# Kernel optimization log

Measured on AMD Instinct MI355X. Metric: run time of the kernel, lower is better.

Reference implementation:

```python
import jax, jax.numpy as jnp
import numpy as np

N_HEAD = 12
N_EMBD = 768

def setup_inputs() -> dict:
    key = jax.random.key(0)
    k1, k2, k3 = jax.random.split(key, 3)
    B, T, C = 4, 2048, N_EMBD
    x = jax.random.normal(k1, (B, T, C), dtype=jnp.float32)
    w_attn = jax.random.normal(k2, (C, 3 * C), dtype=jnp.float32) * (C ** -0.5)
    b_attn = jnp.zeros((3 * C,), dtype=jnp.float32)
    w_proj = jax.random.normal(k3, (C, C), dtype=jnp.float32) * (C ** -0.5)
    b_proj = jnp.zeros((C,), dtype=jnp.float32)
    return {"x": x, "w_attn": w_attn, "b_attn": b_attn, "w_proj": w_proj, "b_proj": b_proj}

def reference(x, w_attn, b_attn, w_proj, b_proj):
    B, T, C = x.shape
    H = N_HEAD
    D = C // H
    qkv = x @ w_attn + b_attn  # [B,T,3C]
    q, k, v = jnp.split(qkv, 3, axis=-1)
    # [B,H,T,D]
    q = q.reshape(B, T, H, D).transpose(0, 2, 1, 3)
    k = k.reshape(B, T, H, D).transpose(0, 2, 1, 3)
    v = v.reshape(B, T, H, D).transpose(0, 2, 1, 3)
    # NOTE: source scales by n_embd**-0.5, not head_dim**-0.5
    scores = jnp.einsum('bhqd,bhkd->bhqk', q, k) * (C ** -0.5)
    causal = jnp.triu(jnp.ones((T, T), dtype=bool), k=1)  # True above diagonal
    scores = jnp.where(causal, -jnp.inf, scores)
    attn = jax.nn.softmax(scores, axis=-1)
    out = jnp.einsum('bhqk,bhkd->bhqd', attn, v)  # [B,H,T,D]
    out = out.transpose(0, 2, 1, 3).reshape(B, T, C)
    return out @ w_proj + b_proj
```

## Files before the change

kernel.cpp:

```cpp
#include <hip/hip_runtime.h>
#include <cstdint>
#include <cstddef>

typedef __attribute__((ext_vector_type(8))) short bf8_t;
typedef __attribute__((ext_vector_type(4))) float f4_t;
typedef __attribute__((ext_vector_type(16))) float f16v_t;
typedef __attribute__((ext_vector_type(2))) unsigned u2_t;
typedef __attribute__((ext_vector_type(4))) unsigned u4_t;

#define DEVFN static __device__ __forceinline__
#define MFMA16(a, b, c) __builtin_amdgcn_mfma_f32_16x16x32_bf16(a, b, c, 0, 0, 0)
#define MFMA32(a, b, c) __builtin_amdgcn_mfma_f32_32x32x16_bf16(a, b, c, 0, 0, 0)

constexpr float kQscale = 0.05205877317700523f;

DEVFN short f2bs(float f) {
  uint32_t u = __builtin_bit_cast(uint32_t, f);
  u = (u + 0x7FFFu + ((u >> 16) & 1u)) >> 16;
  return (short)(uint16_t)u;
}

DEVFN unsigned cvtpk(float lo, float hi) {
  unsigned r;
  asm("v_cvt_pk_bf16_f32 %0, %1, %2" : "=v"(r) : "v"(lo), "v"(hi));
  return r;
}

DEVFN float red2_sum(float v) { return v + __shfl_xor(v, 32, 64); }

DEVFN void gload16(const void* g, void* l) {
  __builtin_amdgcn_global_load_lds(
      (const __attribute__((address_space(1))) void*)g,
      (__attribute__((address_space(3))) void*)l, 16, 0, 0);
}

__global__ __launch_bounds__(256) void prep(const float* __restrict__ x,
                                            short* __restrict__ xb,
                                            const float* __restrict__ w_attn,
                                            short* __restrict__ wat,
                                            const float* __restrict__ w_proj,
                                            short* __restrict__ wpt) {
  __shared__ float tile[32][33];
  const int blk = blockIdx.x, tid = threadIdx.x;
  if (blk < 3072) {
    const int i = blk * 256 + tid;
    const f4_t* p = (const f4_t*)x + (size_t)i * 2;
    f4_t a = p[0], b = p[1];
    bf8_t h;
    h[0] = f2bs(a[0]); h[1] = f2bs(a[1]); h[2] = f2bs(a[2]); h[3] = f2bs(a[3]);
    h[4] = f2bs(b[0]); h[5] = f2bs(b[1]); h[6] = f2bs(b[2]); h[7] = f2bs(b[3]);
    *((bf8_t*)xb + i) = h;
    return;
  }
  const float* w;
  short* wT;
  int N, n0, k0;
  if (blk < 4800) {
    const int bb = blk - 3072;
    w = w_attn; wT = wat; N = 2304;
    n0 = (bb % 72) << 5; k0 = (bb / 72) << 5;
  } else {
    const int bb = blk - 4800;
    w = w_proj; wT = wpt; N = 768;
    n0 = (bb % 24) << 5; k0 = (bb / 24) << 5;
  }
  const int tx = tid & 31, ty = tid >> 5;
#pragma unroll
  for (int i = 0; i < 4; ++i)
    tile[ty * 4 + i][tx] = w[(size_t)(k0 + ty * 4 + i) * N + n0 + tx];
  __syncthreads();
#pragma unroll
  for (int i = 0; i < 4; ++i)
    wT[(size_t)(n0 + ty * 4 + i) * 768 + k0 + tx] = f2bs(tile[tx][ty * 4 + i]);
}

template <int EPI, int BN, int NW>
__global__ __launch_bounds__(NW * 64) void gemm_bf16(
    const short* __restrict__ A, const short* __restrict__ Bt,
    const float* __restrict__ bias, float* __restrict__ outF,
    short* __restrict__ qb, short* __restrict__ kb, short* __restrict__ vtb,
    int Mdim, int Ndim, int Kdim) {
  constexpr int NT = NW * 64;
  constexpr int WCN = NW / 2;
  constexpr int WNW = BN / WCN;
  constexpr int NI = WNW / 16;
  constexpr int ACH = 16 / NW;
  constexpr int BCH = BN / (8 * NW);
  __shared__ char smem[32768 + (BN << 7)];
  const int nbx = gridDim.x;
  const int bid = blockIdx.x + nbx * blockIdx.y;
  const int xcd = bid & 7, slot = bid >> 3;
  const int mp = xcd + ((slot / nbx) << 3);
  const int np = slot % nbx;
  const int m0 = mp << 7, n0 = np * BN;
  const int tid = threadIdx.x;
  const int lane = tid & 63, wid = tid >> 6;
  const int wr = wid / WCN, wc = wid % WCN;
  const int g = lane >> 4, cl = lane & 15;
  const int ldb = Kdim << 1;

  f4_t acc[4][NI];
#pragma unroll
  for (int mi = 0; mi < 4; ++mi)
#pragma unroll
    for (int ni = 0; ni < NI; ++ni) acc[mi][ni] = (f4_t){0.f, 0.f, 0.f, 0.f};

  const char* ga = (const char*)(A + (size_t)m0 * Kdim);
  const char* gb = (const char*)(Bt + (size_t)n0 * Kdim);
  auto stageA = [&](int b, int ks) {
    const int k0b = ks << 7;
    char* Ab = smem + (b << 14);
#pragma unroll
    for (int i = 0; i < ACH; ++i) {
      const int doff = (wid * ACH + i) << 10;
      const int boff = doff + lane * 16;
      const int row = boff >> 7;
      const int src = row * ldb + k0b + ((boff & 127) ^ ((row & 7) << 4));
      gload16(ga + src, Ab + doff);
    }
  };
  auto stageB = [&](int ks) {
    const int k0b = ks << 7;
    char* Bb = smem + 32768;
#pragma unroll
    for (int i = 0; i < BCH; ++i) {
      const int doff = (wid * BCH + i) << 10;
      const int boff = doff + lane * 16;
      const int row = boff >> 7;
      const int src = row * ldb + k0b + ((boff & 127) ^ ((row & 7) << 4));
      gload16(gb + src, Bb + doff);
    }
  };

  const int nk = Kdim >> 6;
  stageA(0, 0);
  stageB(0);
  __syncthreads();

  int cur = 0;
  for (int ks = 0; ks < nk; ++ks) {
    const int ksn = (ks + 1 < nk) ? ks + 1 : ks;
    const char* Ab = smem + (cur << 14);
    const char* Bb = smem + 32768;
    bf8_t bfv[2][NI], af0[4];
#pragma unroll
    for (int kk = 0; kk < 2; ++kk)
#pragma unroll
      for (int ni = 0; ni < NI; ++ni) {
        int lrow = wc * WNW + (ni << 4) + cl;
        bfv[kk][ni] = *(const bf8_t*)&Bb[(lrow << 7) + ((((kk << 2) + g) ^ (lrow & 7)) << 4)];
      }
#pragma unroll
    for (int mi = 0; mi < 4; ++mi) {
      int lrow = (wr << 6) + (mi << 4) + cl;
      af0[mi] = *(const bf8_t*)&Ab[(lrow << 7) + (((g) ^ (lrow & 7)) << 4)];
    }
    __syncthreads();
    stageA(cur ^ 1, ksn);
    stageB(ksn);
#pragma unroll
    for (int mi = 0; mi < 4; ++mi)
#pragma unroll
      for (int ni = 0; ni < NI; ++ni)
        acc[mi][ni] = MFMA16(af0[mi], bfv[0][ni], acc[mi][ni]);
    bf8_t af1[4];
#pragma unroll
    for (int mi = 0; mi < 4; ++mi) {
      int lrow = (wr << 6) + (mi << 4) + cl;
      af1[mi] = *(const bf8_t*)&Ab[(lrow << 7) + (((4 + g) ^ (lrow & 7)) << 4)];
    }
#pragma unroll
    for (int mi = 0; mi < 4; ++mi)
#pragma unroll
      for (int ni = 0; ni < NI; ++ni)
        acc[mi][ni] = MFMA16(af1[mi], bfv[1][ni], acc[mi][ni]);
    __syncthreads();
    cur ^= 1;
  }

  if constexpr (EPI == 1) {
#pragma unroll
    for (int ni = 0; ni < NI; ++ni) {
      const int n = n0 + wc * WNW + (ni << 4) + cl;
      const float bv = bias[n];
#pragma unroll
      for (int mi = 0; mi < 4; ++mi)
#pragma unroll
        for (int r = 0; r < 4; ++r) {
          const int m = m0 + (wr << 6) + (mi << 4) + (g << 2) + r;
          outF[(size_t)m * 768 + n] = acc[mi][ni][r] + bv;
        }
    }
  } else {
    short* T = (short*)smem;
    const int sec = n0 / 768;
    const float qs = (sec == 0) ? kQscale : 1.0f;
#pragma unroll
    for (int ni = 0; ni < NI; ++ni) {
      const int colT = wc * WNW + (ni << 4) + cl;
      const float bv = bias[n0 + colT];
#pragma unroll
      for (int mi = 0; mi < 4; ++mi)
#pragma unroll
        for (int r = 0; r < 4; ++r) {
          const int row = (wr << 6) + (mi << 4) + (g << 2) + r;
          const int colS = ((((colT >> 3) ^ ((row >> 3) & 7)) << 3) | (colT & 7));
          T[row * 132 + colS] = f2bs((acc[mi][ni][r] + bv) * qs);
        }
    }
    __syncthreads();
    if (sec < 2) {
      short* dst0 = (sec == 0) ? qb : kb;
      const int tl = tid & 127;
      const int hh2 = (tid >> 7) & 1;
      const int half = tid >> 8;
      constexpr int JN = (NT == 256) ? 8 : 4;
      const int m = m0 + tl, b = m >> 11, t = m & 2047;
      const int hh = ((n0 - sec * 768) >> 6) + hh2;
      short* dst = dst0 + (size_t)(b * 12 + hh) * 131072 + (size_t)t * 64 + half * 32;
      const int rsw = (tl >> 3) & 7;
#pragma unroll
      for (int j = 0; j < JN; ++j) {
        const int gj = (hh2 << 3) + (half << 2) + j;
        *(bf8_t*)(dst + j * 8) =
            *(const bf8_t*)(T + tl * 132 + ((gj ^ rsw) << 3));
      }
    } else {
      const int chunk = tid & 15;
      constexpr int DLS = NT >> 4;
      const int m = m0 + (chunk << 3);
      const int b = m >> 11, t = m & 2047;
#pragma unroll
      for (int c8 = 0; c8 < 128 / DLS; ++c8) {
        const int dl = (tid >> 4) + c8 * DLS;
        const int nloc = n0 - 1536 + dl;
        const int hh = nloc >> 6, d = nloc & 63;
        const int gsw = ((dl >> 3) ^ (chunk & 7)) << 3;
        bf8_t tmp;
#pragma unroll
        for (int j = 0; j < 8; ++j)
          tmp[j] = T[((chunk << 3) + j) * 132 + gsw + (dl & 7)];
        *(bf8_t*)(vtb + (size_t)(b * 12 + hh) * 131072 + (size_t)d * 2048 + t) = tmp;
      }
    }
  }
}

__global__ __launch_bounds__(256, 2) void attn_fwd(const short* __restrict__ Q,
                                                   const short* __restrict__ K,
                                                   const short* __restrict__ Vt,
                                                   short* __restrict__ O) {
  __shared__ char kv_lds[2][32768];
  const int tid = threadIdx.x;
  const int lane = tid & 63, wid = tid >> 6;
  const int blk = blockIdx.x;
  const int bh = blk % 48;
  const int qg = 15 - blk / 48;
  const int qt = (qg << 2) + wid;
  const int q0 = qt << 5;
  const int col = lane & 31, hi = lane >> 5;

  const short* Qb = Q + (size_t)bh * 131072;
  const short* Kb = K + (size_t)bh * 131072;
  const short* Vb = Vt + (size_t)bh * 131072;

  bf8_t qf[4];
#pragma unroll
  for (int dc = 0; dc < 4; ++dc)
    qf[dc] = *(const bf8_t*)(Qb + (size_t)(q0 + col) * 64 + dc * 16 + hi * 8);

  const f16v_t zf = {0.f,0.f,0.f,0.f,0.f,0.f,0.f,0.f,0.f,0.f,0.f,0.f,0.f,0.f,0.f,0.f};
  f16v_t o0 = zf, o1 = zf;
  float ls[4] = {0.f, 0.f, 0.f, 0.f};

  const int nt = qg + 1;
  const int kxor = (col & 7) << 4;

  auto stage = [&](int b, int kcs) {
    char* buf = &kv_lds[b][0];
    if (wid < 2) {
      const char* g = (const char*)(Kb + (size_t)kcs * 64);
#pragma unroll
      for (int i = 0; i < 8; ++i) {
        const int doff = (wid << 13) + (i << 10);
        const int boff = doff + lane * 16;
        const int src = boff ^ (((boff >> 7) & 7) << 4);
        gload16(g + src, buf + doff);
      }
    } else {
      const char* g = (const char*)Vb + (size_t)kcs * 2;
#pragma unroll
      for (int i = 0; i < 8; ++i) {
        const int doff = ((wid - 2) << 13) + (i << 10);
        const int boff = doff + lane * 16;
        const int row = boff >> 8;
        const int src = row * 4096 + ((boff & 255) ^ ((row & 7) << 4));
        gload16(g + src, buf + 16384 + doff);
      }
    }
  };

  stage(0, 0);
  __syncthreads();

  int cur = 0;
  for (int st = 0; st < nt; ++st) {
    int kcn = (st + 1) << 7;
    if (kcn > 1920) kcn = 1920;
    stage(cur ^ 1, kcn);

#pragma unroll
    for (int h = 0; h < 2; ++h) {
      const int kc = (st << 7) + (h << 6);
      if (kc < q0 + 32) {
        const char* Kl = &kv_lds[cur][h << 13];
        const char* Vl = &kv_lds[cur][16384];
        f16v_t s0 = zf, s1 = zf;
#pragma unroll
        for (int dc = 0; dc < 4; ++dc) {
          const int fo = (dc * 32 + hi * 16) ^ kxor;
          bf8_t k0 = *(const bf8_t*)(Kl + col * 128 + fo);
          bf8_t k1 = *(const bf8_t*)(Kl + (32 + col) * 128 + fo);
          __builtin_amdgcn_s_setprio(1);
          s0 = MFMA32(k0, qf[dc], s0);
          s1 = MFMA32(k1, qf[dc], s1);
          __builtin_amdgcn_s_setprio(0);
        }
        if (kc + 63 > q0) {
          const int qq = q0 + col;
#pragma unroll
          for (int r = 0; r < 16; ++r) {
            const int kb_ = kc + (r & 3) + 8 * (r >> 2) + 4 * hi;
            if (kb_ > qq) s0[r] = -1e30f;
            if (kb_ + 32 > qq) s1[r] = -1e30f;
          }
        }
#pragma unroll
        for (int r = 0; r < 16; ++r) {
          s0[r] = __builtin_amdgcn_exp2f(s0[r]);
          s1[r] = __builtin_amdgcn_exp2f(s1[r]);
        }
#pragma unroll
        for (int r = 0; r < 4; ++r)
          ls[r] += ((s0[r] + s0[r + 4]) + (s0[r + 8] + s0[r + 12])) +
                   ((s1[r] + s1[r + 4]) + (s1[r + 8] + s1[r + 12]));
#pragma unroll
        for (int c = 0; c < 4; ++c) {
          const int b8 = (c & 1) * 8;
          float p0, p1, p2, p3, p4, p5, p6, p7;
          if (c < 2) {
            p0 = s0[b8+0]; p1 = s0[b8+1]; p2 = s0[b8+2]; p3 = s0[b8+3];
            p4 = s0[b8+4]; p5 = s0[b8+5]; p6 = s0[b8+6]; p7 = s0[b8+7];
          } else {
            p0 = s1[b8+0]; p1 = s1[b8+1]; p2 = s1[b8+2]; p3 = s1[b8+3];
            p4 = s1[b8+4]; p5 = s1[b8+5]; p6 = s1[b8+6]; p7 = s1[b8+7];
          }
          unsigned w0 = cvtpk(p0, p1), w1 = cvtpk(p2, p3);
          unsigned w2 = cvtpk(p4, p5), w3 = cvtpk(p6, p7);
          u2_t ra = __builtin_amdgcn_permlane32_swap(w0, w2, false, false);
          u2_t rb = __builtin_amdgcn_permlane32_swap(w1, w3, false, false);
          const bf8_t pf = __builtin_bit_cast(bf8_t, (u4_t){ra[0], rb[0], ra[1], rb[1]});
          const int vo = ((h << 7) + c * 32 + hi * 16) ^ kxor;
          bf8_t v0 = *(const bf8_t*)(Vl + col * 256 + vo);
          bf8_t v1 = *(const bf8_t*)(Vl + (32 + col) * 256 + vo);
          __builtin_amdgcn_s_setprio(1);
          o0 = MFMA32(v0, pf, o0);
          o1 = MFMA32(v1, pf, o1);
          __builtin_amdgcn_s_setprio(0);
        }
      }
    }
    __syncthreads();
    cur ^= 1;
  }

  const float l = red2_sum((ls[0] + ls[1]) + (ls[2] + ls[3]));
  const float rl = 1.0f / l;
  const int b_ = bh / 12, hh = bh % 12;
  short* Op = O + (size_t)b_ * 2048 * 768 + (size_t)(q0 + col) * 768 + hh * 64;
#pragma unroll
  for (int rq = 0; rq < 4; ++rq) {
    u2_t w0, w1;
    w0[0] = cvtpk(o0[4*rq+0] * rl, o0[4*rq+1] * rl);
    w0[1] = cvtpk(o0[4*rq+2] * rl, o0[4*rq+3] * rl);
    w1[0] = cvtpk(o1[4*rq+0] * rl, o1[4*rq+1] * rl);
    w1[1] = cvtpk(o1[4*rq+2] * rl, o1[4*rq+3] * rl);
    *(u2_t*)(Op + rq * 8 + hi * 4) = w0;
    *(u2_t*)(Op + 32 + rq * 8 + hi * 4) = w1;
  }
}

extern "C" void kernel_launch(void* const* d_in, const int* in_sizes, int n_in,
                              void* d_out, int out_size, void* d_ws, size_t ws_size,
                              hipStream_t stream) {
  const float* x      = (const float*)d_in[0];
  const float* w_attn = (const float*)d_in[1];
  const float* b_attn = (const float*)d_in[2];
  const float* w_proj = (const float*)d_in[3];
  const float* b_proj = (const float*)d_in[4];
  float* out = (float*)d_out;

  const size_t QSZ = (size_t)4 * 12 * 2048 * 64;
  short* ws  = (short*)d_ws;
  short* qb  = ws;
  short* kb  = qb + QSZ;
  short* vtb = kb + QSZ;
  short* xb  = vtb + QSZ;
  short* ob  = xb;
  short* wat = xb + QSZ;
  short* wpt = wat + (size_t)2304 * 768;

  prep<<<5376, 256, 0, stream>>>(x, xb, w_attn, wat, w_proj, wpt);

  gemm_bf16<0, 128, 8><<<dim3(18, 64), 512, 0, stream>>>(xb, wat, b_attn, nullptr,
                                                         qb, kb, vtb, 8192, 2304, 768);
  attn_fwd<<<768, 256, 0, stream>>>(qb, kb, vtb, ob);
  gemm_bf16<1, 64, 8><<<dim3(12, 64), 512, 0, stream>>>(ob, wpt, b_proj, out,
                                                        nullptr, nullptr, nullptr, 8192, 768, 768);
}
```

Measured before the change: 114.8 us.

## Single-buffer GEMM LDS, batch MFMA with raised priority, widen attention blocks to 8 waves

The GEMM drops the double-buffered A tile in favour of a single LDS buffer to shrink shared memory and raise occupancy. It now loads both k-halves of A and B fragments up front and issues all MFMAs under s_setprio. The attention kernel moves to 512-thread blocks covering 256 query rows, so each K/V tile staged in LDS is shared by twice as many waves and the grid halves. Costs: GEMM loads now overlap less with compute, causal work per block is coarser and less balanced, and the 2-blocks-per-CU launch bound is dropped.

New measurement: 121.0 us. 5.4% more time.

```diff
diff --git a/kernel.cpp b/kernel.cpp
--- a/kernel.cpp
+++ b/kernel.cpp
@@ -86,7 +86,9 @@
   constexpr int NI = WNW / 16;
   constexpr int ACH = 16 / NW;
   constexpr int BCH = BN / (8 * NW);
-  __shared__ char smem[32768 + (BN << 7)];
+  constexpr int SST = 16384 + (BN << 7);
+  constexpr int SSZ = (EPI == 0 && SST < 33792) ? 33792 : SST;
+  __shared__ char smem[SSZ];
   const int nbx = gridDim.x;
   const int bid = blockIdx.x + nbx * blockIdx.y;
   const int xcd = bid & 7, slot = bid >> 3;
@@ -107,75 +109,65 @@
 
   const char* ga = (const char*)(A + (size_t)m0 * Kdim);
   const char* gb = (const char*)(Bt + (size_t)n0 * Kdim);
-  auto stageA = [&](int b, int ks) {
+  auto stageA = [&](int ks) {
     const int k0b = ks << 7;
-    char* Ab = smem + (b << 14);
 #pragma unroll
     for (int i = 0; i < ACH; ++i) {
       const int doff = (wid * ACH + i) << 10;
       const int boff = doff + lane * 16;
       const int row = boff >> 7;
       const int src = row * ldb + k0b + ((boff & 127) ^ ((row & 7) << 4));
-      gload16(ga + src, Ab + doff);
+      gload16(ga + src, smem + doff);
     }
   };
   auto stageB = [&](int ks) {
     const int k0b = ks << 7;
-    char* Bb = smem + 32768;
 #pragma unroll
     for (int i = 0; i < BCH; ++i) {
       const int doff = (wid * BCH + i) << 10;
       const int boff = doff + lane * 16;
       const int row = boff >> 7;
       const int src = row * ldb + k0b + ((boff & 127) ^ ((row & 7) << 4));
-      gload16(gb + src, Bb + doff);
+      gload16(gb + src, smem + 16384 + doff);
     }
   };
 
   const int nk = Kdim >> 6;
-  stageA(0, 0);
+  stageA(0);
   stageB(0);
   __syncthreads();
 
-  int cur = 0;
   for (int ks = 0; ks < nk; ++ks) {
     const int ksn = (ks + 1 < nk) ? ks + 1 : ks;
-    const char* Ab = smem + (cur << 14);
-    const char* Bb = smem + 32768;
-    bf8_t bfv[2][NI], af0[4];
-#pragma unroll
-    for (int kk = 0; kk < 2; ++kk)
+    const char* Ab = smem;
+    const char* Bb = smem + 16384;
+    bf8_t bfv[2][NI], afv[2][4];
+#pragma unroll
+    for (int kk = 0; kk < 2; ++kk) {
 #pragma unroll
       for (int ni = 0; ni < NI; ++ni) {
         int lrow = wc * WNW + (ni << 4) + cl;
         bfv[kk][ni] = *(const bf8_t*)&Bb[(lrow << 7) + ((((kk << 2) + g) ^ (lrow & 7)) << 4)];
       }
 #pragma unroll
-    for (int mi = 0; mi < 4; ++mi) {
-      int lrow = (wr << 6) + (mi << 4) + cl;
-      af0[mi] = *(const bf8_t*)&Ab[(lrow << 7) + (((g) ^ (lrow & 7)) << 4)];
+      for (int mi = 0; mi < 4; ++mi) {
+        int lrow = (wr << 6) + (mi << 4) + cl;
+        afv[kk][mi] = *(const bf8_t*)&Ab[(lrow << 7) + ((((kk << 2) + g) ^ (lrow & 7)) << 4)];
+      }
     }
     __syncthreads();
-    stageA(cur ^ 1, ksn);
+    stageA(ksn);
     stageB(ksn);
-#pragma unroll
-    for (int mi = 0; mi < 4; ++mi)
-#pragma unroll
-      for (int ni = 0; ni < NI; ++ni)
-        acc[mi][ni] = MFMA16(af0[mi], bfv[0][ni], acc[mi][ni]);
-    bf8_t af1[4];
-#pragma unroll
-    for (int mi = 0; mi < 4; ++mi) {
-      int lrow = (wr << 6) + (mi << 4) + cl;
-      af1[mi] = *(const bf8_t*)&Ab[(lrow << 7) + (((4 + g) ^ (lrow & 7)) << 4)];
-    }
-#pragma unroll
-    for (int mi = 0; mi < 4; ++mi)
-#pragma unroll
-      for (int ni = 0; ni < NI; ++ni)
-        acc[mi][ni] = MFMA16(af1[mi], bfv[1][ni], acc[mi][ni]);
+    __builtin_amdgcn_s_setprio(1);
+#pragma unroll
+    for (int kk = 0; kk < 2; ++kk)
+#pragma unroll
+      for (int mi = 0; mi < 4; ++mi)
+#pragma unroll
+        for (int ni = 0; ni < NI; ++ni)
+          acc[mi][ni] = MFMA16(afv[kk][mi], bfv[kk][ni], acc[mi][ni]);
+    __builtin_amdgcn_s_setprio(0);
     __syncthreads();
-    cur ^= 1;
   }
 
   if constexpr (EPI == 1) {
@@ -195,6 +187,7 @@
     short* T = (short*)smem;
     const int sec = n0 / 768;
     const float qs = (sec == 0) ? kQscale : 1.0f;
+    __syncthreads();
 #pragma unroll
     for (int ni = 0; ni < NI; ++ni) {
       const int colT = wc * WNW + (ni << 4) + cl;
@@ -246,17 +239,17 @@
   }
 }
 
-__global__ __launch_bounds__(256, 2) void attn_fwd(const short* __restrict__ Q,
-                                                   const short* __restrict__ K,
-                                                   const short* __restrict__ Vt,
-                                                   short* __restrict__ O) {
+__global__ __launch_bounds__(512) void attn_fwd(const short* __restrict__ Q,
+                                                const short* __restrict__ K,
+                                                const short* __restrict__ Vt,
+                                                short* __restrict__ O) {
   __shared__ char kv_lds[2][32768];
   const int tid = threadIdx.x;
   const int lane = tid & 63, wid = tid >> 6;
   const int blk = blockIdx.x;
   const int bh = blk % 48;
-  const int qg = 15 - blk / 48;
-  const int qt = (qg << 2) + wid;
+  const int qg = 7 - blk / 48;
+  const int qt = (qg << 3) + wid;
   const int q0 = qt << 5;
   const int col = lane & 31, hi = lane >> 5;
 
@@ -273,16 +266,16 @@
   f16v_t o0 = zf, o1 = zf;
   float ls[4] = {0.f, 0.f, 0.f, 0.f};
 
-  const int nt = qg + 1;
+  const int nt = (qg << 1) + 2;
   const int kxor = (col & 7) << 4;
 
   auto stage = [&](int b, int kcs) {
     char* buf = &kv_lds[b][0];
-    if (wid < 2) {
+    if (wid < 4) {
       const char* g = (const char*)(Kb + (size_t)kcs * 64);
 #pragma unroll
-      for (int i = 0; i < 8; ++i) {
-        const int doff = (wid << 13) + (i << 10);
+      for (int i = 0; i < 4; ++i) {
+        const int doff = (wid << 12) + (i << 10);
         const int boff = doff + lane * 16;
         const int src = boff ^ (((boff >> 7) & 7) << 4);
         gload16(g + src, buf + doff);
@@ -290,8 +283,8 @@
     } else {
       const char* g = (const char*)Vb + (size_t)kcs * 2;
 #pragma unroll
-      for (int i = 0; i < 8; ++i) {
-        const int doff = ((wid - 2) << 13) + (i << 10);
+      for (int i = 0; i < 4; ++i) {
+        const int doff = ((wid - 4) << 12) + (i << 10);
         const int boff = doff + lane * 16;
         const int row = boff >> 8;
         const int src = row * 4096 + ((boff & 255) ^ ((row & 7) << 4));
@@ -414,7 +407,7 @@
 
   gemm_bf16<0, 128, 8><<<dim3(18, 64), 512, 0, stream>>>(xb, wat, b_attn, nullptr,
                                                          qb, kb, vtb, 8192, 2304, 768);
-  attn_fwd<<<768, 256, 0, stream>>>(qb, kb, vtb, ob);
+  attn_fwd<<<384, 512, 0, stream>>>(qb, kb, vtb, ob);
   gemm_bf16<1, 64, 8><<<dim3(12, 64), 512, 0, stream>>>(ob, wpt, b_proj, out,
                                                         nullptr, nullptr, nullptr, 8192, 768, 768);
 }
```
